# Kernel optimization log

Measured on AMD Instinct MI355X. Metric: run time of the kernel, lower is better.

## Reference

```python
import jax, jax.numpy as jnp
import numpy as np

NUM_HEADS = 16
HIDDEN = 2048
HEAD_SIZE = HIDDEN // NUM_HEADS        # 128
ROTARY_PCT = 0.25
ROTARY_DIM = int(HEAD_SIZE * ROTARY_PCT)  # 32
ROTARY_BASE = 10000.0
BATCH = 4
SEQ = 1024
TOTAL = BATCH * SEQ


def setup_inputs() -> dict:
    key = jax.random.key(0)
    k1, k2, k3 = jax.random.split(key, 3)
    hidden_states = jax.random.normal(k1, (TOTAL, HIDDEN), dtype=jnp.float32)
    w_qkv = jax.random.normal(k2, (3 * HIDDEN, HIDDEN), dtype=jnp.float32) * (HIDDEN ** -0.5)
    b_qkv = jnp.zeros((3 * HIDDEN,), dtype=jnp.float32)
    w_dense = jax.random.normal(k3, (HIDDEN, HIDDEN), dtype=jnp.float32) * (HIDDEN ** -0.5)
    b_dense = jnp.zeros((HIDDEN,), dtype=jnp.float32)
    layer_past = jnp.zeros((TOTAL, 2, NUM_HEADS, HEAD_SIZE), dtype=jnp.float32)
    position_ids = jnp.tile(jnp.arange(SEQ, dtype=jnp.int64), BATCH)
    cu_seqlens = (jnp.arange(BATCH + 1, dtype=jnp.int32) * SEQ)
    return {
        "hidden_states": hidden_states, "layer_past": layer_past,
        "w_qkv": w_qkv, "b_qkv": b_qkv, "w_dense": w_dense, "b_dense": b_dense,
        "position_ids": position_ids, "cu_seqlens": cu_seqlens,
        "max_s": SEQ, "prefill": 1,
    }


def _apply_rotary(x, cos, sin):
    # x: [T, h, d]; GPT-NeoX (rotate-half, non-interleaved) on first ROTARY_DIM dims
    x_rot, x_pass = x[..., :ROTARY_DIM], x[..., ROTARY_DIM:]
    half = ROTARY_DIM // 2
    x1, x2 = x_rot[..., :half], x_rot[..., half:]
    return jnp.concatenate([x1 * cos - x2 * sin, x1 * sin + x2 * cos, x_pass], axis=-1)


def reference(hidden_states, layer_past, w_qkv, b_qkv, w_dense, b_dense,
              position_ids, cu_seqlens, max_s, prefill):
    # QKV projection: [T, 3H]
    qkv = hidden_states @ w_qkv.T + b_qkv
    # rearrange '... (h three d)' then permute -> [T, 3, h, d]
    qkv = qkv.reshape(TOTAL, NUM_HEADS, 3, HEAD_SIZE).transpose(0, 2, 1, 3)

    # rotary cos/sin per token position: [T, 1, ROTARY_DIM/2]
    inv_freq = 1.0 / (ROTARY_BASE ** (jnp.arange(0, ROTARY_DIM, 2, dtype=jnp.float32) / ROTARY_DIM))
    freqs = position_ids.astype(jnp.float32)[:, None] * inv_freq[None, :]
    cos = jnp.cos(freqs)[:, None, :]
    sin = jnp.sin(freqs)[:, None, :]

    q = _apply_rotary(qkv[:, 0], cos, sin)   # [T, h, d]
    k = _apply_rotary(qkv[:, 1], cos, sin)
    v = qkv[:, 2]

    # prefill: cache write layer_past[...] = kv_rot (byproduct, not returned here)
    # ragged causal flash attention; all sequences have equal length SEQ here
    qb = q.reshape(BATCH, SEQ, NUM_HEADS, HEAD_SIZE)
    kb = k.reshape(BATCH, SEQ, NUM_HEADS, HEAD_SIZE)
    vb = v.reshape(BATCH, SEQ, NUM_HEADS, HEAD_SIZE)

    scale = HEAD_SIZE ** -0.5
    scores = jnp.einsum('bqhd,bkhd->bhqk', qb, kb) * scale  # [B, h, S, S]
    causal = jnp.tril(jnp.ones((SEQ, SEQ), dtype=bool))
    scores = jnp.where(causal[None, None], scores, jnp.finfo(scores.dtype).min)
    probs = jax.nn.softmax(scores, axis=-1)
    attn = jnp.einsum('bhqk,bkhd->bqhd', probs, vb)          # [B, S, h, d]
    attn = attn.reshape(TOTAL, HIDDEN)

    return attn @ w_dense.T + b_dense
```

## Files before the change

kernel.cpp:

```cpp
#include <hip/hip_runtime.h>
#include <stdint.h>

#define NUM_HEADS 16
#define HIDDEN    2048
#define HEAD_SIZE 128
#define TOTAL     4096
#define SEQ       1024
#define QKV_N     (3*HIDDEN)

typedef __bf16 bf16x8 __attribute__((ext_vector_type(8)));
typedef float  f32x4  __attribute__((ext_vector_type(4)));

__device__ __forceinline__ unsigned short f2bf(float f) {
  unsigned u = __float_as_uint(f);
  u += 0x7FFFu + ((u >> 16) & 1u);
  return (unsigned short)(u >> 16);
}
__device__ __forceinline__ float bf2f(unsigned short h) {
  return __uint_as_float(((unsigned)h) << 16);
}
__device__ __forceinline__ void cp16(void* lds, const void* g) {
  __builtin_amdgcn_global_load_lds(
      (const __attribute__((address_space(1))) void*)g,
      (__attribute__((address_space(3))) void*)lds, 16, 0, 0);
}

__global__ __launch_bounds__(256) void f32_to_bf16_multi(
    const float* __restrict__ a, unsigned short* __restrict__ oa, int na,
    const float* __restrict__ b, unsigned short* __restrict__ ob, int nb,
    const float* __restrict__ c, unsigned short* __restrict__ oc, int nc)
{
  int i = (blockIdx.x * 256 + threadIdx.x) * 4;
  const float* src; unsigned short* dst;
  if (i < na)            { src = a; dst = oa; }
  else if (i < na + nb)  { i -= na; src = b; dst = ob; }
  else                   { i -= na + nb; if (i >= nc) return; src = c; dst = oc; }
  float4 v = *(const float4*)(src + i);
  unsigned p0 = (unsigned)f2bf(v.x) | ((unsigned)f2bf(v.y) << 16);
  unsigned p1 = (unsigned)f2bf(v.z) | ((unsigned)f2bf(v.w) << 16);
  uint2 pk; pk.x = p0; pk.y = p1;
  *(uint2*)(dst + i) = pk;
}

__global__ __launch_bounds__(256, 2) void gemm_qkv(
    const unsigned short* __restrict__ A,
    const unsigned short* __restrict__ B,
    const float* __restrict__ bias,
    const int* __restrict__ pos_ids,
    unsigned short* __restrict__ Qb,
    unsigned short* __restrict__ Kb,
    unsigned short* __restrict__ Vt,
    int M, int N, int K)
{
  __shared__ unsigned short lsA[2][128*32];
  __shared__ unsigned short lsB[2][256*32];
  const int tid  = threadIdx.x;
  const int w    = tid >> 6, lane = tid & 63;
  const int quad = lane >> 4, lm = lane & 15;
  const int wm   = w >> 1, wn = w & 1;
  const int mBase = blockIdx.y * 128;
  const int nBase = blockIdx.x * 256;
  const int swz = (lm >> 1) & 3;

  const f32x4 zero4 = {0.f, 0.f, 0.f, 0.f};
  f32x4 acc[4][8];
#pragma unroll
  for (int i = 0; i < 4; i++)
#pragma unroll
    for (int j = 0; j < 8; j++) acc[i][j] = zero4;

  const int cg = ((tid & 3) ^ ((tid >> 3) & 3)) * 16;

  auto stage = [&](int bufi, int k0) {
#pragma unroll
    for (int i = 0; i < 2; i++) {
      int off = i * 4096 + tid * 16;
      int row = off >> 6;
      cp16((char*)&lsA[bufi][0] + off, (const char*)(A + (size_t)(mBase + row) * K + k0) + cg);
    }
#pragma unroll
    for (int i = 0; i < 4; i++) {
      int off = i * 4096 + tid * 16;
      int row = off >> 6;
      cp16((char*)&lsB[bufi][0] + off, (const char*)(B + (size_t)(nBase + row) * K + k0) + cg);
    }
  };

  int buf = 0;
  stage(0, 0);

  for (int k0 = 0; k0 < K; k0 += 32) {
    __syncthreads();
    bf16x8 af[4], bfr[8];
#pragma unroll
    for (int mf = 0; mf < 4; mf++)
      af[mf] = *(const bf16x8*)(&lsA[buf][(wm * 64 + mf * 16 + lm) * 32 + (quad ^ swz) * 8]);
#pragma unroll
    for (int nf = 0; nf < 8; nf++)
      bfr[nf] = *(const bf16x8*)(&lsB[buf][(wn * 128 + nf * 16 + lm) * 32 + (quad ^ swz) * 8]);
    if (k0 + 32 < K) stage(buf ^ 1, k0 + 32);
#pragma unroll
    for (int mf = 0; mf < 4; mf++)
#pragma unroll
      for (int nf = 0; nf < 8; nf++)
        acc[mf][nf] = __builtin_amdgcn_mfma_f32_16x16x32_bf16(af[mf], bfr[nf], acc[mf][nf], 0, 0, 0);
    buf ^= 1;
  }

  const int col0 = nBase + wn * 128;
  const int chunk = col0 >> 7;
  const int hh = chunk / 3, t = chunk - 3 * hh;
  if (t == 2) {
#pragma unroll
    for (int nf = 0; nf < 8; nf++) {
      int d = nf * 16 + lm;
      float bv = bias[col0 + d];
#pragma unroll
      for (int mf = 0; mf < 4; mf++) {
        int row0 = mBase + wm * 64 + mf * 16 + quad * 4;
        int b = row0 >> 10, s0 = row0 & 1023;
        unsigned u0 = (unsigned)f2bf(acc[mf][nf][0] + bv) | ((unsigned)f2bf(acc[mf][nf][1] + bv) << 16);
        unsigned u1 = (unsigned)f2bf(acc[mf][nf][2] + bv) | ((unsigned)f2bf(acc[mf][nf][3] + bv) << 16);
        uint2 pk; pk.x = u0; pk.y = u1;
        *(uint2*)(Vt + ((size_t)(b * NUM_HEADS + hh) * HEAD_SIZE + d) * SEQ + s0) = pk;
      }
    }
  } else {
    unsigned short* dst = (t == 0) ? Qb : Kb;
    {
      const float inv = exp2f(-0.8304820237f * (float)lm);
      const float bv0 = bias[col0 + lm];
      const float bv1 = bias[col0 + 16 + lm];
#pragma unroll
      for (int mf = 0; mf < 4; mf++) {
        int row0 = mBase + wm * 64 + mf * 16 + quad * 4;
#pragma unroll
        for (int r = 0; r < 4; r++) {
          int row = row0 + r;
          int b = row >> 10, s = row & 1023;
          float pos = (float)pos_ids[row];
          float sn, cs;
          sincosf(pos * inv, &sn, &cs);
          float x1 = acc[mf][0][r] + bv0;
          float x2 = acc[mf][1][r] + bv1;
          size_t rb = ((size_t)(b * NUM_HEADS + hh) * SEQ + s) * HEAD_SIZE;
          dst[rb + lm]      = f2bf(x1 * cs - x2 * sn);
          dst[rb + 16 + lm] = f2bf(x1 * sn + x2 * cs);
        }
      }
    }
#pragma unroll
    for (int nf = 2; nf < 8; nf++) {
      int d = nf * 16 + lm;
      float bv = bias[col0 + d];
#pragma unroll
      for (int mf = 0; mf < 4; mf++) {
        int row0 = mBase + wm * 64 + mf * 16 + quad * 4;
#pragma unroll
        for (int r = 0; r < 4; r++) {
          int row = row0 + r;
          int b = row >> 10, s = row & 1023;
          dst[((size_t)(b * NUM_HEADS + hh) * SEQ + s) * HEAD_SIZE + d] = f2bf(acc[mf][nf][r] + bv);
        }
      }
    }
  }
}

__global__ __launch_bounds__(256) void gemm_dense(
    const unsigned short* __restrict__ A,
    const unsigned short* __restrict__ B,
    const float* __restrict__ bias,
    float* __restrict__ Cf,
    int M, int N, int K)
{
  __shared__ unsigned short lsA[2][128*32];
  __shared__ unsigned short lsB[2][128*32];
  const int tid  = threadIdx.x;
  const int w    = tid >> 6, lane = tid & 63;
  const int quad = lane >> 4, lm = lane & 15;
  const int wm   = w & 1, wn = w >> 1;
  const int mBase = blockIdx.y * 128;
  const int nBase = blockIdx.x * 128;
  const int swz = (lm >> 1) & 3;

  const f32x4 zero4 = {0.f, 0.f, 0.f, 0.f};
  f32x4 acc[4][4];
#pragma unroll
  for (int i = 0; i < 4; i++)
#pragma unroll
    for (int j = 0; j < 4; j++) acc[i][j] = zero4;

  const int cg = ((tid & 3) ^ ((tid >> 3) & 3)) * 16;

  auto stage = [&](int bufi, int k0) {
#pragma unroll
    for (int i = 0; i < 2; i++) {
      int off = i * 4096 + tid * 16;
      int row = off >> 6;
      cp16((char*)&lsA[bufi][0] + off, (const char*)(A + (size_t)(mBase + row) * K + k0) + cg);
    }
#pragma unroll
    for (int i = 0; i < 2; i++) {
      int off = i * 4096 + tid * 16;
      int row = off >> 6;
      cp16((char*)&lsB[bufi][0] + off, (const char*)(B + (size_t)(nBase + row) * K + k0) + cg);
    }
  };

  int buf = 0;
  stage(0, 0);

  for (int k0 = 0; k0 < K; k0 += 32) {
    __syncthreads();
    bf16x8 af[4], bfr[4];
#pragma unroll
    for (int mf = 0; mf < 4; mf++)
      af[mf] = *(const bf16x8*)(&lsA[buf][(wm * 64 + mf * 16 + lm) * 32 + (quad ^ swz) * 8]);
#pragma unroll
    for (int nf = 0; nf < 4; nf++)
      bfr[nf] = *(const bf16x8*)(&lsB[buf][(wn * 64 + nf * 16 + lm) * 32 + (quad ^ swz) * 8]);
    if (k0 + 32 < K) stage(buf ^ 1, k0 + 32);
#pragma unroll
    for (int mf = 0; mf < 4; mf++)
#pragma unroll
      for (int nf = 0; nf < 4; nf++)
        acc[mf][nf] = __builtin_amdgcn_mfma_f32_16x16x32_bf16(af[mf], bfr[nf], acc[mf][nf], 0, 0, 0);
    buf ^= 1;
  }

#pragma unroll
  for (int nf = 0; nf < 4; nf++) {
    int col = nBase + wn * 64 + nf * 16 + lm;
    float bv = bias[col];
#pragma unroll
    for (int mf = 0; mf < 4; mf++) {
      int row0 = mBase + wm * 64 + mf * 16 + quad * 4;
#pragma unroll
      for (int r = 0; r < 4; r++)
        Cf[(size_t)(row0 + r) * N + col] = acc[mf][nf][r] + bv;
    }
  }
}

__global__ __launch_bounds__(256, 2) void flash_attn_k(
    const unsigned short* __restrict__ Q,
    const unsigned short* __restrict__ K,
    const unsigned short* __restrict__ VT,
    unsigned short* __restrict__ O)
{
  const int bh = blockIdx.x;
  const int pair = blockIdx.y;
  const int qa = 15 - pair, qb = pair;
  const int b = bh >> 4, h = bh & 15;
  const size_t base = (size_t)bh * SEQ * HEAD_SIZE;
  const unsigned short* Qp = Q + base;
  const unsigned short* Kp = K + base;
  const unsigned short* Vp = VT + base;

  __shared__ unsigned short Ks[2][4][64*32];
  __shared__ unsigned short Vl[2][128*64];
  __shared__ unsigned short Ps[64][72];

  const int tid  = threadIdx.x;
  const int w    = tid >> 6, lane = tid & 63;
  const int quad = lane >> 4, lm = lane & 15;
  const int swz4 = (lm >> 1) & 3;
  const int swz8 = lm & 7;
  const int cgK = ((tid & 3) ^ ((tid >> 3) & 3)) * 8;
  const int cgV = ((tid & 7) ^ ((tid >> 3) & 7)) * 8;

  const float K1 = 0.1275156876f;
  const f32x4 zero4 = {0.f, 0.f, 0.f, 0.f};
  const __bf16 one = (__bf16)1.0f;
  const bf16x8 vones = {one, one, one, one, one, one, one, one};

  auto stage = [&](int buf, int kt) {
    const unsigned short* krow = Kp + (size_t)(kt * 64 + (tid >> 2)) * HEAD_SIZE + cgK;
#pragma unroll
    for (int kk = 0; kk < 4; kk++)
      cp16((char*)&Ks[buf][kk][0] + tid * 16, krow + kk * 32);
#pragma unroll
    for (int i = 0; i < 4; i++) {
      int off = i * 4096 + tid * 16;
      int d = off >> 7;
      cp16((char*)&Vl[buf][0] + off, Vp + (size_t)d * SEQ + kt * 64 + cgV);
    }
  };

  int buf = 0;
  stage(0, 0);

  for (int ph = 0; ph < 2; ph++) {
    const int qt = ph ? qb : qa;
    bf16x8 qf[4];
    {
      const unsigned short* qrow = Qp + (size_t)(qt * 64 + w * 16 + lm) * HEAD_SIZE;
#pragma unroll
      for (int kk = 0; kk < 4; kk++)
        qf[kk] = *(const bf16x8*)(qrow + kk * 32 + quad * 8);
    }
    float m_r[4];
#pragma unroll
    for (int r = 0; r < 4; r++) m_r[r] = -1e30f;
    f32x4 lacc = zero4;
    f32x4 o[8];
#pragma unroll
    for (int i = 0; i < 8; i++) o[i] = zero4;

    for (int kt = 0; kt <= qt; ++kt) {
      __syncthreads();
      bool last = (ph == 1) && (kt == qt);
      if (!last) stage(buf ^ 1, (kt < qt) ? kt + 1 : 0);

      f32x4 sf[4];
#pragma unroll
      for (int nf = 0; nf < 4; nf++) {
        f32x4 accs = zero4;
#pragma unroll
        for (int kk = 0; kk < 4; kk++) {
          bf16x8 kfrag = *(const bf16x8*)(&Ks[buf][kk][(nf * 16 + lm) * 32 + (quad ^ swz4) * 8]);
          accs = __builtin_amdgcn_mfma_f32_16x16x32_bf16(qf[kk], kfrag, accs, 0, 0, 0);
        }
        sf[nf] = accs;
      }
      if (kt == qt) {
        int qrow0 = qt * 64 + w * 16 + quad * 4;
#pragma unroll
        for (int nf = 0; nf < 4; nf++) {
          int col = kt * 64 + nf * 16 + lm;
#pragma unroll
          for (int r = 0; r < 4; r++)
            if (col > qrow0 + r) sf[nf][r] = -1e30f;
        }
      }
      float alpha[4];
#pragma unroll
      for (int r = 0; r < 4; r++) {
        float v = fmaxf(fmaxf(sf[0][r], sf[1][r]), fmaxf(sf[2][r], sf[3][r]));
        v = fmaxf(v, __shfl_xor(v, 1));
        v = fmaxf(v, __shfl_xor(v, 2));
        v = fmaxf(v, __shfl_xor(v, 4));
        v = fmaxf(v, __shfl_xor(v, 8));
        float mn = fmaxf(m_r[r], v);
        alpha[r] = exp2f((m_r[r] - mn) * K1);
        m_r[r] = mn;
      }
#pragma unroll
      for (int nf = 0; nf < 4; nf++)
#pragma unroll
        for (int r = 0; r < 4; r++) {
          float p = exp2f((sf[nf][r] - m_r[r]) * K1);
          Ps[w * 16 + quad * 4 + r][nf * 16 + lm] = f2bf(p);
        }
#pragma unroll
      for (int df = 0; df < 8; df++)
#pragma unroll
        for (int r = 0; r < 4; r++) o[df][r] *= alpha[r];
#pragma unroll
      for (int r = 0; r < 4; r++) lacc[r] *= alpha[r];

#pragma unroll
      for (int ks = 0; ks < 2; ks++) {
        bf16x8 pf = *(const bf16x8*)(&Ps[w * 16 + lm][ks * 32 + quad * 8]);
        lacc = __builtin_amdgcn_mfma_f32_16x16x32_bf16(pf, vones, lacc, 0, 0, 0);
#pragma unroll
        for (int df = 0; df < 8; df++) {
          bf16x8 vf = *(const bf16x8*)(&Vl[buf][(df * 16 + lm) * 64 + (((ks * 4 + quad) ^ swz8)) * 8]);
          o[df] = __builtin_amdgcn_mfma_f32_16x16x32_bf16(pf, vf, o[df], 0, 0, 0);
        }
      }
      buf ^= 1;
    }

    float rl[4];
#pragma unroll
    for (int r = 0; r < 4; r++) rl[r] = 1.f / lacc[r];
    int row0 = b * SEQ + qt * 64 + w * 16 + quad * 4;
#pragma unroll
    for (int df = 0; df < 8; df++) {
      int col = h * HEAD_SIZE + df * 16 + lm;
#pragma unroll
      for (int r = 0; r < 4; r++)
        O[(size_t)(row0 + r) * HIDDEN + col] = f2bf(o[df][r] * rl[r]);
    }
  }
}

extern "C" void kernel_launch(void* const* d_in, const int* in_sizes, int n_in,
                              void* d_out, int out_size, void* d_ws, size_t ws_size,
                              hipStream_t stream)
{
  const float* hs   = (const float*)d_in[0];
  const float* wqkv = (const float*)d_in[2];
  const float* bqkv = (const float*)d_in[3];
  const float* wd   = (const float*)d_in[4];
  const float* bd   = (const float*)d_in[5];
  const int*   pos  = (const int*)d_in[6];

  char* ws = (char*)d_ws;
  unsigned short* hsb = (unsigned short*)ws;  ws += (size_t)TOTAL * HIDDEN * 2;
  unsigned short* wqb = (unsigned short*)ws;  ws += (size_t)QKV_N * HIDDEN * 2;
  unsigned short* wdb = (unsigned short*)ws;  ws += (size_t)HIDDEN * HIDDEN * 2;
  unsigned short* Qb  = (unsigned short*)ws;  ws += (size_t)TOTAL * HIDDEN * 2;
  unsigned short* Kb  = (unsigned short*)ws;  ws += (size_t)TOTAL * HIDDEN * 2;
  unsigned short* Vt  = (unsigned short*)ws;  ws += (size_t)TOTAL * HIDDEN * 2;
  unsigned short* attnb = hsb;
  if (ws_size < (size_t)(ws - (char*)d_ws)) return;

  const int na = TOTAL * HIDDEN, nb = QKV_N * HIDDEN, nc = HIDDEN * HIDDEN;
  f32_to_bf16_multi<<<(na + nb + nc) / 1024, 256, 0, stream>>>(
      hs, hsb, na, wqkv, wqb, nb, wd, wdb, nc);

  gemm_qkv<<<dim3(QKV_N / 256, TOTAL / 128), 256, 0, stream>>>(
      hsb, wqb, bqkv, pos, Qb, Kb, Vt, TOTAL, QKV_N, HIDDEN);

  flash_attn_k<<<dim3(64, 8), 256, 0, stream>>>(Qb, Kb, Vt, attnb);

  gemm_dense<<<dim3(HIDDEN / 128, TOTAL / 128), 256, 0, stream>>>(
      attnb, wdb, bd, (float*)d_out, TOTAL, HIDDEN, HIDDEN);
}
```

Baseline: 384.9 us.

## Rewrite QKV GEMM as 256x256 tile, 8-phase pipelined kernel with 512 threads

```diff
diff --git a/kernel.cpp b/kernel.cpp
--- a/kernel.cpp
+++ b/kernel.cpp
@@ -42,82 +42,182 @@
   *(uint2*)(dst + i) = pk;
 }
 
-__global__ __launch_bounds__(256, 2) void gemm_qkv(
+#define SBAR()   __builtin_amdgcn_sched_barrier(0)
+#define HBAR()   __builtin_amdgcn_s_barrier()
+#define WLGKM0() asm volatile("s_waitcnt lgkmcnt(0)" ::: "memory")
+#define WVMC(n)  asm volatile("s_waitcnt vmcnt(" #n ")" ::: "memory")
+#define PH_SYNC() do { SBAR(); HBAR(); WLGKM0(); SBAR(); } while (0)
+#define PH_END()  do { SBAR(); HBAR(); } while (0)
+
+__device__ __forceinline__ void stage2(char* lb, const char* sb, int o0, int o1,
+                                       size_t gg0, size_t gg1) {
+  cp16(lb + o0, sb + gg0);
+  cp16(lb + o1, sb + gg1);
+}
+
+template<int MH>
+__device__ __forceinline__ void ldA4(bf16x8 (&d)[4][2], const unsigned short* ls,
+                                     int base, int ch0) {
+#pragma unroll
+  for (int mi = 0; mi < 4; mi++) {
+    d[mi][0] = *(const bf16x8*)((const char*)ls + base + (MH*4 + mi)*2048 + ch0);
+    d[mi][1] = *(const bf16x8*)((const char*)ls + base + (MH*4 + mi)*2048 + (ch0 ^ 64));
+  }
+}
+template<int NH>
+__device__ __forceinline__ void ldB2(bf16x8 (&d)[2][2], const unsigned short* ls,
+                                     int base, int ch0) {
+#pragma unroll
+  for (int ni = 0; ni < 2; ni++) {
+    d[ni][0] = *(const bf16x8*)((const char*)ls + base + (NH*2 + ni)*2048 + ch0);
+    d[ni][1] = *(const bf16x8*)((const char*)ls + base + (NH*2 + ni)*2048 + (ch0 ^ 64));
+  }
+}
+template<int MH, int NH>
+__device__ __forceinline__ void mfmaQ(f32x4 (&acc)[8][4], const bf16x8 (&AF)[4][2],
+                                      const bf16x8 (&BF)[2][2]) {
+  __builtin_amdgcn_s_setprio(1);
+#pragma unroll
+  for (int kk = 0; kk < 2; kk++)
+#pragma unroll
+    for (int mi = 0; mi < 4; mi++)
+#pragma unroll
+      for (int ni = 0; ni < 2; ni++)
+        acc[MH*4 + mi][NH*2 + ni] = __builtin_amdgcn_mfma_f32_16x16x32_bf16(
+            AF[mi][kk], BF[ni][kk], acc[MH*4 + mi][NH*2 + ni], 0, 0, 0);
+  __builtin_amdgcn_s_setprio(0);
+}
+
+__global__ __launch_bounds__(512, 2) void gemm_qkv_8ph(
     const unsigned short* __restrict__ A,
     const unsigned short* __restrict__ B,
     const float* __restrict__ bias,
     const int* __restrict__ pos_ids,
     unsigned short* __restrict__ Qb,
     unsigned short* __restrict__ Kb,
-    unsigned short* __restrict__ Vt,
-    int M, int N, int K)
+    unsigned short* __restrict__ Vt)
 {
-  __shared__ unsigned short lsA[2][128*32];
-  __shared__ unsigned short lsB[2][256*32];
+  __shared__ unsigned short lsA[2][256*64];
+  __shared__ unsigned short lsB[2][256*64];
+
   const int tid  = threadIdx.x;
   const int w    = tid >> 6, lane = tid & 63;
   const int quad = lane >> 4, lm = lane & 15;
-  const int wm   = w >> 1, wn = w & 1;
-  const int mBase = blockIdx.y * 128;
-  const int nBase = blockIdx.x * 256;
-  const int swz = (lm >> 1) & 3;
+  const int wm   = w >> 2, wn = w & 3;
+
+  const int g  = ((int)blockIdx.x & 7) * 48 + ((int)blockIdx.x >> 3);
+  const int my = g & 15, nx = g >> 4;
+  const int mBase = my * 256, nBase = nx * 256;
+
+  const int off0 = tid * 16;
+  const int off1 = off0 + 8192;
+  const int r0 = off0 >> 7, r1 = off1 >> 7;
+  const size_t g0 = (size_t)r0 * (HIDDEN*2) + ((((off0 >> 4) & 7) ^ (r0 & 7)) << 4);
+  const size_t g1 = (size_t)r1 * (HIDDEN*2) + ((((off1 >> 4) & 7) ^ (r1 & 7)) << 4);
+  const char* Abase = (const char*)A + (size_t)mBase * HIDDEN * 2;
+  const char* Bbase = (const char*)B + (size_t)nBase * HIDDEN * 2;
+
+  const int ch0   = ((quad ^ (lm & 7)) << 4);
+  const int aBase = (wm * 128 + lm) * 128;
+  const int bBase = (wn * 64  + lm) * 128;
+
+#define STG(bi, h, t) stage2( \
+    (((h) < 2) ? (char*)&lsA[bi][0] : (char*)&lsB[bi][0]) + (((h) & 1) * 16384), \
+    (((h) < 2) ? Abase : Bbase) + (size_t)((h) & 1) * (128 * HIDDEN * 2) + (size_t)(t) * 128, \
+    off0, off1, g0, g1)
 
   const f32x4 zero4 = {0.f, 0.f, 0.f, 0.f};
-  f32x4 acc[4][8];
-#pragma unroll
-  for (int i = 0; i < 4; i++)
-#pragma unroll
-    for (int j = 0; j < 8; j++) acc[i][j] = zero4;
-
-  const int cg = ((tid & 3) ^ ((tid >> 3) & 3)) * 16;
-
-  auto stage = [&](int bufi, int k0) {
-#pragma unroll
-    for (int i = 0; i < 2; i++) {
-      int off = i * 4096 + tid * 16;
-      int row = off >> 6;
-      cp16((char*)&lsA[bufi][0] + off, (const char*)(A + (size_t)(mBase + row) * K + k0) + cg);
-    }
-#pragma unroll
-    for (int i = 0; i < 4; i++) {
-      int off = i * 4096 + tid * 16;
-      int row = off >> 6;
-      cp16((char*)&lsB[bufi][0] + off, (const char*)(B + (size_t)(nBase + row) * K + k0) + cg);
-    }
-  };
-
-  int buf = 0;
-  stage(0, 0);
-
-  for (int k0 = 0; k0 < K; k0 += 32) {
-    __syncthreads();
-    bf16x8 af[4], bfr[8];
-#pragma unroll
-    for (int mf = 0; mf < 4; mf++)
-      af[mf] = *(const bf16x8*)(&lsA[buf][(wm * 64 + mf * 16 + lm) * 32 + (quad ^ swz) * 8]);
-#pragma unroll
-    for (int nf = 0; nf < 8; nf++)
-      bfr[nf] = *(const bf16x8*)(&lsB[buf][(wn * 128 + nf * 16 + lm) * 32 + (quad ^ swz) * 8]);
-    if (k0 + 32 < K) stage(buf ^ 1, k0 + 32);
-#pragma unroll
-    for (int mf = 0; mf < 4; mf++)
-#pragma unroll
-      for (int nf = 0; nf < 8; nf++)
-        acc[mf][nf] = __builtin_amdgcn_mfma_f32_16x16x32_bf16(af[mf], bfr[nf], acc[mf][nf], 0, 0, 0);
-    buf ^= 1;
-  }
-
-  const int col0 = nBase + wn * 128;
+  f32x4 acc[8][4];
+#pragma unroll
+  for (int i = 0; i < 8; i++)
+#pragma unroll
+    for (int j = 0; j < 4; j++) acc[i][j] = zero4;
+
+  bf16x8 a0[4][2], a1[4][2], b0[2][2], b1[2][2];
+
+  STG(0, 0, 0); STG(0, 1, 0); STG(0, 2, 0); STG(0, 3, 0);
+  STG(1, 0, 1); STG(1, 1, 1);
+  WVMC(4);
+  SBAR(); HBAR();
+
+#pragma unroll 1
+  for (int t = 0; t < 30; t += 2) {
+    ldA4<0>(a0, &lsA[0][0], aBase, ch0);
+    ldB2<0>(b0, &lsB[0][0], bBase, ch0);
+    STG(1, 2, t + 1);
+    PH_SYNC(); mfmaQ<0,0>(acc, a0, b0); PH_END();
+
+    ldA4<1>(a1, &lsA[0][0], aBase, ch0);
+    STG(1, 3, t + 1);
+    PH_SYNC(); mfmaQ<1,0>(acc, a1, b0); PH_END();
+
+    ldB2<1>(b1, &lsB[0][0], bBase, ch0);
+    STG(0, 0, t + 2);
+    PH_SYNC(); mfmaQ<0,1>(acc, a0, b1); PH_END();
+
+    STG(0, 1, t + 2);
+    WVMC(4);
+    PH_SYNC(); mfmaQ<1,1>(acc, a1, b1); PH_END();
+
+    ldA4<0>(a0, &lsA[1][0], aBase, ch0);
+    ldB2<0>(b0, &lsB[1][0], bBase, ch0);
+    STG(0, 2, t + 2);
+    PH_SYNC(); mfmaQ<0,0>(acc, a0, b0); PH_END();
+
+    ldA4<1>(a1, &lsA[1][0], aBase, ch0);
+    STG(0, 3, t + 2);
+    PH_SYNC(); mfmaQ<1,0>(acc, a1, b0); PH_END();
+
+    ldB2<1>(b1, &lsB[1][0], bBase, ch0);
+    STG(1, 0, t + 3);
+    PH_SYNC(); mfmaQ<0,1>(acc, a0, b1); PH_END();
+
+    STG(1, 1, t + 3);
+    WVMC(4);
+    PH_SYNC(); mfmaQ<1,1>(acc, a1, b1); PH_END();
+  }
+
+  ldA4<0>(a0, &lsA[0][0], aBase, ch0);
+  ldB2<0>(b0, &lsB[0][0], bBase, ch0);
+  STG(1, 2, 31);
+  PH_SYNC(); mfmaQ<0,0>(acc, a0, b0); PH_END();
+
+  ldA4<1>(a1, &lsA[0][0], aBase, ch0);
+  STG(1, 3, 31);
+  PH_SYNC(); mfmaQ<1,0>(acc, a1, b0); PH_END();
+
+  ldB2<1>(b1, &lsB[0][0], bBase, ch0);
+  PH_SYNC(); mfmaQ<0,1>(acc, a0, b1); PH_END();
+
+  WVMC(0);
+  PH_SYNC(); mfmaQ<1,1>(acc, a1, b1); PH_END();
+
+  ldA4<0>(a0, &lsA[1][0], aBase, ch0);
+  ldB2<0>(b0, &lsB[1][0], bBase, ch0);
+  PH_SYNC(); mfmaQ<0,0>(acc, a0, b0); PH_END();
+
+  ldA4<1>(a1, &lsA[1][0], aBase, ch0);
+  PH_SYNC(); mfmaQ<1,0>(acc, a1, b0); PH_END();
+
+  ldB2<1>(b1, &lsB[1][0], bBase, ch0);
+  PH_SYNC(); mfmaQ<0,1>(acc, a0, b1); PH_END();
+
+  PH_SYNC(); mfmaQ<1,1>(acc, a1, b1);
+#undef STG
+
+  const int col0  = nBase + wn * 64;
   const int chunk = col0 >> 7;
-  const int hh = chunk / 3, t = chunk - 3 * hh;
-  if (t == 2) {
-#pragma unroll
-    for (int nf = 0; nf < 8; nf++) {
-      int d = nf * 16 + lm;
-      float bv = bias[col0 + d];
-#pragma unroll
-      for (int mf = 0; mf < 4; mf++) {
-        int row0 = mBase + wm * 64 + mf * 16 + quad * 4;
+  const int hh = chunk / 3, tq = chunk - 3 * hh;
+  const int dbase = col0 & 127;
+
+  if (tq == 2) {
+#pragma unroll
+    for (int nf = 0; nf < 4; nf++) {
+      int d = dbase + nf * 16 + lm;
+      float bv = bias[col0 + nf * 16 + lm];
+#pragma unroll
+      for (int mf = 0; mf < 8; mf++) {
+        int row0 = mBase + wm * 128 + mf * 16 + quad * 4;
         int b = row0 >> 10, s0 = row0 & 1023;
         unsigned u0 = (unsigned)f2bf(acc[mf][nf][0] + bv) | ((unsigned)f2bf(acc[mf][nf][1] + bv) << 16);
         unsigned u1 = (unsigned)f2bf(acc[mf][nf][2] + bv) | ((unsigned)f2bf(acc[mf][nf][3] + bv) << 16);
@@ -126,14 +226,14 @@
       }
     }
   } else {
-    unsigned short* dst = (t == 0) ? Qb : Kb;
-    {
+    unsigned short* dst = (tq == 0) ? Qb : Kb;
+    if (dbase == 0) {
       const float inv = exp2f(-0.8304820237f * (float)lm);
       const float bv0 = bias[col0 + lm];
       const float bv1 = bias[col0 + 16 + lm];
 #pragma unroll
-      for (int mf = 0; mf < 4; mf++) {
-        int row0 = mBase + wm * 64 + mf * 16 + quad * 4;
+      for (int mf = 0; mf < 8; mf++) {
+        int row0 = mBase + wm * 128 + mf * 16 + quad * 4;
 #pragma unroll
         for (int r = 0; r < 4; r++) {
           int row = row0 + r;
@@ -148,19 +248,35 @@
           dst[rb + 16 + lm] = f2bf(x1 * sn + x2 * cs);
         }
       }
-    }
-#pragma unroll
-    for (int nf = 2; nf < 8; nf++) {
-      int d = nf * 16 + lm;
-      float bv = bias[col0 + d];
-#pragma unroll
-      for (int mf = 0; mf < 4; mf++) {
-        int row0 = mBase + wm * 64 + mf * 16 + quad * 4;
-#pragma unroll
-        for (int r = 0; r < 4; r++) {
-          int row = row0 + r;
-          int b = row >> 10, s = row & 1023;
-          dst[((size_t)(b * NUM_HEADS + hh) * SEQ + s) * HEAD_SIZE + d] = f2bf(acc[mf][nf][r] + bv);
+#pragma unroll
+      for (int nf = 2; nf < 4; nf++) {
+        int d = nf * 16 + lm;
+        float bv = bias[col0 + d];
+#pragma unroll
+        for (int mf = 0; mf < 8; mf++) {
+          int row0 = mBase + wm * 128 + mf * 16 + quad * 4;
+#pragma unroll
+          for (int r = 0; r < 4; r++) {
+            int row = row0 + r;
+            int b = row >> 10, s = row & 1023;
+            dst[((size_t)(b * NUM_HEADS + hh) * SEQ + s) * HEAD_SIZE + d] = f2bf(acc[mf][nf][r] + bv);
+          }
+        }
+      }
+    } else {
+#pragma unroll
+      for (int nf = 0; nf < 4; nf++) {
+        int d = 64 + nf * 16 + lm;
+        float bv = bias[col0 + nf * 16 + lm];
+#pragma unroll
+        for (int mf = 0; mf < 8; mf++) {
+          int row0 = mBase + wm * 128 + mf * 16 + quad * 4;
+#pragma unroll
+          for (int r = 0; r < 4; r++) {
+            int row = row0 + r;
+            int b = row >> 10, s = row & 1023;
+            dst[((size_t)(b * NUM_HEADS + hh) * SEQ + s) * HEAD_SIZE + d] = f2bf(acc[mf][nf][r] + bv);
+          }
         }
       }
     }
@@ -412,8 +528,7 @@
   f32_to_bf16_multi<<<(na + nb + nc) / 1024, 256, 0, stream>>>(
       hs, hsb, na, wqkv, wqb, nb, wd, wdb, nc);
 
-  gemm_qkv<<<dim3(QKV_N / 256, TOTAL / 128), 256, 0, stream>>>(
-      hsb, wqb, bqkv, pos, Qb, Kb, Vt, TOTAL, QKV_N, HIDDEN);
+  gemm_qkv_8ph<<<dim3(384), 512, 0, stream>>>(hsb, wqb, bqkv, pos, Qb, Kb, Vt);
 
   flash_attn_k<<<dim3(64, 8), 256, 0, stream>>>(Qb, Kb, Vt, attnb);
 
```

Measured after the change: 398.6 us. +3.5%, slower.
